# Optimization experiments

Hardware: AMD Instinct MI355X
Metric: run time of the kernel (lower is better)

Reference implementation:

```python
import jax, jax.numpy as jnp
import numpy as np

N, E, F_IN, H, L = 1536, 49152, 27, 64, 32


def _ln(x, g, b, eps=1e-5):
    m = x.mean(-1, keepdims=True)
    v = ((x - m) ** 2).mean(-1, keepdims=True)
    return (x - m) * jax.lax.rsqrt(v + eps) * g + b


def _gatv2(x, src, dst, Wl, bl, Wr, br, att, bias, n):
    # PyG GATv2Conv, heads=1: alpha_ij = softmax_j( att . leaky_relu(Wl x_j + Wr x_i) )
    xl = x @ Wl + bl  # source transform [n,H]
    xr = x @ Wr + br  # target transform [n,H]
    e = jax.nn.leaky_relu(xl[src] + xr[dst], 0.2)  # [E',H]
    s = e @ att  # [E'] attention logits
    m = jax.ops.segment_max(s, dst, num_segments=n)
    w = jnp.exp(s - m[dst])
    denom = jax.ops.segment_sum(w, dst, num_segments=n)
    alpha = w / denom[dst]
    return jax.ops.segment_sum(alpha[:, None] * xl[src], dst, num_segments=n) + bias


def _model(x, eps_nodes, eps_graph, edge_index,
           Wl1, bl1, Wr1, br1, att1, bias1,
           Wl2, bl2, Wr2, br2, att2, bias2,
           Wnm, bnm, Wnv, bnv, Wgm, bgm, Wgv, bgv,
           Wd1, bd1, ln1_g, ln1_b, Wd2, bd2, ln2_g, ln2_b, Wd3, bd3,
           We1, be1, lne_g, lne_b, We2, be2,
           Wf1, bf1, lnf_g, lnf_b, Wf2, bf2):
    n = x.shape[0]
    loop = jnp.arange(n)
    src = jnp.concatenate([edge_index[0], loop])  # add self loops (PyG default)
    dst = jnp.concatenate([edge_index[1], loop])
    h = jax.nn.relu(_gatv2(x, src, dst, Wl1, bl1, Wr1, br1, att1, bias1, n))
    h = jax.nn.relu(_gatv2(h, src, dst, Wl2, bl2, Wr2, br2, att2, bias2, n))
    node_mu = h @ Wnm + bnm
    node_logvar = h @ Wnv + bnv
    gh = h.mean(0)
    graph_mu = gh @ Wgm + bgm
    graph_logvar = gh @ Wgv + bgv
    z = node_mu + eps_nodes * jnp.exp(0.5 * node_logvar)  # node reparam (training)
    _zg = graph_mu + eps_graph * jnp.exp(0.5 * graph_logvar)  # z_graph: computed, unused downstream as in source
    # dec_node_features MLP
    nf = _ln(jax.nn.relu(z @ Wd1 + bd1), ln1_g, ln1_b)
    nf = _ln(jax.nn.relu(nf @ Wd2 + bd2), ln2_g, ln2_b)
    nf = nf @ Wd3 + bd3  # [n, F_IN]
    # feature_refinement (node_embeddings = h is passed in forward)
    nf = _ln(jax.nn.relu(jnp.concatenate([nf, h], -1) @ Wf1 + bf1), lnf_g, lnf_b)
    node_features = nf @ Wf2 + bf2
    # edge_pred over all i<j pairs, vectorized (replaces the O(N^2) python loop)
    iu, ju = jnp.triu_indices(n, k=1)
    ei = jnp.concatenate([z[iu], z[ju]], -1)  # [P, 2L]
    eh = _ln(jax.nn.relu(ei @ We1 + be1), lne_g, lne_b)
    edge_logits = (eh @ We2 + be2)[:, 0]  # [P]
    return node_features, edge_logits, node_mu, node_logvar, graph_mu, graph_logvar


def setup_inputs() -> dict:
    key = jax.random.key(0)
    ki = iter(jax.random.split(key, 40))
    def W(fi, fo):
        return jax.random.normal(next(ki), (fi, fo), jnp.float32) / np.sqrt(fi)
    z64 = jnp.zeros((H,), jnp.float32)
    o64 = jnp.ones((H,), jnp.float32)
    zL = jnp.zeros((L,), jnp.float32)
    zF = jnp.zeros((F_IN,), jnp.float32)
    inp = {}
    inp["x"] = jax.random.normal(next(ki), (N, F_IN), jnp.float32)
    inp["edge_index"] = jax.random.randint(next(ki), (2, E), 0, N)
    inp["eps_nodes"] = jax.random.normal(next(ki), (N, L), jnp.float32)
    inp["eps_graph"] = jax.random.normal(next(ki), (L,), jnp.float32)
    inp.update(Wl1=W(F_IN, H), bl1=z64, Wr1=W(F_IN, H), br1=z64,
               att1=jax.random.normal(next(ki), (H,), jnp.float32) / np.sqrt(H), bias1=z64,
               Wl2=W(H, H), bl2=z64, Wr2=W(H, H), br2=z64,
               att2=jax.random.normal(next(ki), (H,), jnp.float32) / np.sqrt(H), bias2=z64)
    inp.update(Wnm=W(H, L), bnm=zL, Wnv=W(H, L), bnv=zL,
               Wgm=W(H, L), bgm=zL, Wgv=W(H, L), bgv=zL)
    inp.update(Wd1=W(L, H), bd1=z64, ln1_g=o64, ln1_b=z64,
               Wd2=W(H, H), bd2=z64, ln2_g=o64, ln2_b=z64,
               Wd3=W(H, F_IN), bd3=zF)
    inp.update(We1=W(2 * L, H), be1=z64, lne_g=o64, lne_b=z64,
               We2=W(H, 1), be2=jnp.zeros((1,), jnp.float32))
    inp.update(Wf1=W(F_IN + H, H), bf1=z64, lnf_g=o64, lnf_b=z64,
               Wf2=W(H, F_IN), bf2=zF)
    return inp


def reference(x, edge_index, eps_nodes, eps_graph,
              Wl1, bl1, Wr1, br1, att1, bias1,
              Wl2, bl2, Wr2, br2, att2, bias2,
              Wnm, bnm, Wnv, bnv, Wgm, bgm, Wgv, bgv,
              Wd1, bd1, ln1_g, ln1_b, Wd2, bd2, ln2_g, ln2_b, Wd3, bd3,
              We1, be1, lne_g, lne_b, We2, be2,
              Wf1, bf1, lnf_g, lnf_b, Wf2, bf2):
    return _model(x, eps_nodes, eps_graph, edge_index,
                  Wl1, bl1, Wr1, br1, att1, bias1,
                  Wl2, bl2, Wr2, br2, att2, bias2,
                  Wnm, bnm, Wnv, bnv, Wgm, bgm, Wgv, bgv,
                  Wd1, bd1, ln1_g, ln1_b, Wd2, bd2, ln2_g, ln2_b, Wd3, bd3,
                  We1, be1, lne_g, lne_b, We2, be2,
                  Wf1, bf1, lnf_g, lnf_b, Wf2, bf2)
```

## Files before the change

### kernel.cpp

```cpp
#include <hip/hip_runtime.h>

#define NN 1536
#define NE 49152
#define NM (NE + NN)
#define FIN 27
#define HD 64
#define LDIM 32
#define PP 1178880

#define EL_OFF  (NN*FIN)
#define MU_OFF  (EL_OFF + PP)
#define LV_OFF  (MU_OFF + NN*LDIM)
#define GMU_OFF (LV_OFF + NN*LDIM)
#define GLV_OFF (GMU_OFF + LDIM)

#define EP_BLOCKS 1024

__device__ __forceinline__ float wsum(float v) {
#pragma unroll
  for (int m = 1; m < 64; m <<= 1) v += __shfl_xor(v, m, 64);
  return v;
}
__device__ __forceinline__ void wsum2(float& a, float& b) {
#pragma unroll
  for (int m = 1; m < 64; m <<= 1) {
    a += __shfl_xor(a, m, 64);
    b += __shfl_xor(b, m, 64);
  }
}
__device__ __forceinline__ float lnorm64(float x, float g, float b) {
  float s1 = x, s2 = x * x;
  wsum2(s1, s2);
  float mu = s1 * (1.0f / 64.0f);
  float var = fmaf(-mu, mu, s2 * (1.0f / 64.0f));
  return (x - mu) * rsqrtf(var + 1e-5f) * g + b;
}
__device__ __forceinline__ void cp4(float* dst, const float* __restrict__ src,
                                    int n4, int t) {
  const float4* s4 = (const float4*)src;
  float4* d4 = (float4*)dst;
  for (int e = t; e < n4; e += 256) d4[e] = s4[e];
}

template <int KIN, bool FUSE, bool ZERO>
__global__ __launch_bounds__(256) void gvae_xform(
    const float* __restrict__ in, const float* __restrict__ Dn,
    const float* __restrict__ hbias,
    const float* __restrict__ Wl, const float* __restrict__ bl,
    const float* __restrict__ Wr, const float* __restrict__ br,
    float* __restrict__ xl, float* __restrict__ xr,
    float* __restrict__ zbase, int nz4) {
  __shared__ __align__(16) float sWl[KIN * HD];
  __shared__ __align__(16) float sWr[KIN * HD];
  int t = threadIdx.x;
  if (ZERO) {
    float4 zz = {0.f, 0.f, 0.f, 0.f};
    float4* z4 = (float4*)zbase;
    for (int e = blockIdx.x * 256 + t; e < nz4; e += (NN / 4) * 256) z4[e] = zz;
  }
  cp4(sWl, Wl, KIN * 16, t);
  cp4(sWr, Wr, KIN * 16, t);
  int i = blockIdx.x * 4 + (t >> 6);
  int k = t & 63;
  float xv = (k < KIN) ? in[i * KIN + k] : 0.f;
  if (FUSE) xv = fmaxf(xv / Dn[i] + hbias[k], 0.f);
  float l0 = bl[k], l1 = 0.f, r0 = br[k], r1 = 0.f;
  __syncthreads();
#pragma unroll
  for (int a = 0; a < KIN; a += 2) {
    float xa = __shfl(xv, a, 64);
    l0 = fmaf(xa, sWl[a * HD + k], l0);
    r0 = fmaf(xa, sWr[a * HD + k], r0);
    if (a + 1 < KIN) {
      float xb = __shfl(xv, a + 1, 64);
      l1 = fmaf(xb, sWl[(a + 1) * HD + k], l1);
      r1 = fmaf(xb, sWr[(a + 1) * HD + k], r1);
    }
  }
  xl[i * HD + k] = l0 + l1;
  xr[i * HD + k] = r0 + r1;
}

__global__ __launch_bounds__(256) void gvae_edgepass(
    const int* __restrict__ ei,
    const float* __restrict__ xl, const float* __restrict__ xr,
    const float* __restrict__ att,
    float* __restrict__ A, float* __restrict__ D) {
  int wid = blockIdx.x * 4 + (threadIdx.x >> 6);
  int lane = threadIdx.x & 63;
  const int NW = EP_BLOCKS * 4;
  float ak = att[lane];
#pragma unroll 2
  for (int m = wid; m < NM; m += NW) {
    int src, dst;
    if (m < NE) { src = ei[m]; dst = ei[NE + m]; }
    else        { src = m - NE; dst = src; }
    float xls = xl[src * HD + lane];
    float e = xls + xr[dst * HD + lane];
    e = fmaxf(e, 0.2f * e);
    float w = expf(wsum(e * ak));
    atomicAdd(&A[dst * HD + lane], w * xls);
    if (lane == 0) atomicAdd(&D[dst], w);
  }
}

#define oE1 0
#define oD1 4096
#define oD2 6144
#define oF1 10240
#define SWTOT 16064

__global__ __launch_bounds__(256, 2) void gvae_node(
    const float* __restrict__ A2, const float* __restrict__ D2,
    const float* __restrict__ bias2,
    const float* __restrict__ eps,
    const float* __restrict__ Wnm, const float* __restrict__ bnm,
    const float* __restrict__ Wnv, const float* __restrict__ bnv,
    const float* __restrict__ We1, const float* __restrict__ be1,
    const float* __restrict__ Wd1, const float* __restrict__ bd1,
    const float* __restrict__ g1, const float* __restrict__ b1,
    const float* __restrict__ Wd2, const float* __restrict__ bd2,
    const float* __restrict__ g2, const float* __restrict__ b2,
    const float* __restrict__ Wd3, const float* __restrict__ bd3,
    const float* __restrict__ Wf1, const float* __restrict__ bf1,
    const float* __restrict__ gf, const float* __restrict__ bfv,
    const float* __restrict__ Wf2, const float* __restrict__ bf2,
    float* __restrict__ uo, float* __restrict__ vo,
    float* __restrict__ gh, float* __restrict__ out) {
  __shared__ __align__(16) float sW[SWTOT];
  __shared__ float ghred[256];
  int t = threadIdx.x;
  cp4(sW + oE1, We1, 1024, t);
  cp4(sW + oD1, Wd1, 512, t);
  cp4(sW + oD2, Wd2, 1024, t);
  cp4(sW + oF1, Wf1, 1456, t);

  int i = blockIdx.x * 4 + (t >> 6);
  int k = t & 63;
  int kk = k & 31;
  int kc = (k < FIN) ? k : (FIN - 1);
  float h2k = fmaxf(A2[i * HD + k] / D2[i] + bias2[k], 0.f);
  ghred[t] = h2k;
  __syncthreads();
  if (t < 64) {
    float s = (ghred[t] + ghred[t + 64]) + (ghred[t + 128] + ghred[t + 192]);
    atomicAdd(&gh[t], s * (1.0f / NN));
  }

  const float* W = (k < 32) ? Wnm : Wnv;
  float c0 = (k < 32) ? bnm[kk] : bnv[kk];
  float c1 = 0.f, c2 = 0.f, c3 = 0.f;
#pragma unroll
  for (int a = 0; a < HD; a += 4) {
    c0 = fmaf(__shfl(h2k, a, 64),     W[a * LDIM + kk],       c0);
    c1 = fmaf(__shfl(h2k, a + 1, 64), W[(a + 1) * LDIM + kk], c1);
    c2 = fmaf(__shfl(h2k, a + 2, 64), W[(a + 2) * LDIM + kk], c2);
    c3 = fmaf(__shfl(h2k, a + 3, 64), W[(a + 3) * LDIM + kk], c3);
  }
  float acc = (c0 + c1) + (c2 + c3);
  if (k < 32) out[MU_OFF + i * LDIM + kk] = acc;
  else        out[LV_OFF + i * LDIM + kk] = acc;

  float lv = __shfl(acc, k + 32, 64);
  float zk = acc + eps[i * LDIM + kk] * expf(0.5f * lv);

  float u0 = be1[k], u1 = 0.f, v0 = 0.f, v1 = 0.f;
#pragma unroll
  for (int a = 0; a < LDIM; a += 2) {
    float za = __shfl(zk, a, 64);
    float zb = __shfl(zk, a + 1, 64);
    u0 = fmaf(za, sW[oE1 + a * HD + k], u0);
    u1 = fmaf(zb, sW[oE1 + (a + 1) * HD + k], u1);
    v0 = fmaf(za, sW[oE1 + (a + LDIM) * HD + k], v0);
    v1 = fmaf(zb, sW[oE1 + (a + 1 + LDIM) * HD + k], v1);
  }
  uo[i * HD + k] = u0 + u1;
  vo[i * HD + k] = v0 + v1;

  c0 = bd1[k]; c1 = 0.f; c2 = 0.f; c3 = 0.f;
#pragma unroll
  for (int a = 0; a < LDIM; a += 4) {
    c0 = fmaf(__shfl(zk, a, 64),     sW[oD1 + a * HD + k],       c0);
    c1 = fmaf(__shfl(zk, a + 1, 64), sW[oD1 + (a + 1) * HD + k], c1);
    c2 = fmaf(__shfl(zk, a + 2, 64), sW[oD1 + (a + 2) * HD + k], c2);
    c3 = fmaf(__shfl(zk, a + 3, 64), sW[oD1 + (a + 3) * HD + k], c3);
  }
  float nf1 = lnorm64(fmaxf((c0 + c1) + (c2 + c3), 0.f), g1[k], b1[k]);

  c0 = bd2[k]; c1 = 0.f; c2 = 0.f; c3 = 0.f;
#pragma unroll
  for (int a = 0; a < HD; a += 4) {
    c0 = fmaf(__shfl(nf1, a, 64),     sW[oD2 + a * HD + k],       c0);
    c1 = fmaf(__shfl(nf1, a + 1, 64), sW[oD2 + (a + 1) * HD + k], c1);
    c2 = fmaf(__shfl(nf1, a + 2, 64), sW[oD2 + (a + 2) * HD + k], c2);
    c3 = fmaf(__shfl(nf1, a + 3, 64), sW[oD2 + (a + 3) * HD + k], c3);
  }
  float nf2 = lnorm64(fmaxf((c0 + c1) + (c2 + c3), 0.f), g2[k], b2[k]);

  c0 = 0.f; c1 = 0.f; c2 = 0.f; c3 = 0.f;
#pragma unroll
  for (int a = 0; a < HD; a += 4) {
    c0 = fmaf(__shfl(nf2, a, 64),     Wd3[a * FIN + kc],       c0);
    c1 = fmaf(__shfl(nf2, a + 1, 64), Wd3[(a + 1) * FIN + kc], c1);
    c2 = fmaf(__shfl(nf2, a + 2, 64), Wd3[(a + 2) * FIN + kc], c2);
    c3 = fmaf(__shfl(nf2, a + 3, 64), Wd3[(a + 3) * FIN + kc], c3);
  }
  float nf3 = (k < FIN) ? ((c0 + c1) + (c2 + c3) + bd3[kc]) : 0.f;

  c0 = bf1[k]; c1 = 0.f; c2 = 0.f; c3 = 0.f;
#pragma unroll
  for (int j = 0; j < FIN; j++) {
    float nj = __shfl(nf3, j, 64);
    c0 = fmaf(nj, sW[oF1 + j * HD + k], c0);
  }
#pragma unroll
  for (int a = 0; a < HD; a += 4) {
    c0 = fmaf(__shfl(h2k, a, 64),     sW[oF1 + (FIN + a) * HD + k],     c0);
    c1 = fmaf(__shfl(h2k, a + 1, 64), sW[oF1 + (FIN + a + 1) * HD + k], c1);
    c2 = fmaf(__shfl(h2k, a + 2, 64), sW[oF1 + (FIN + a + 2) * HD + k], c2);
    c3 = fmaf(__shfl(h2k, a + 3, 64), sW[oF1 + (FIN + a + 3) * HD + k], c3);
  }
  float rr = lnorm64(fmaxf((c0 + c1) + (c2 + c3), 0.f), gf[k], bfv[k]);

  c0 = 0.f; c1 = 0.f; c2 = 0.f; c3 = 0.f;
#pragma unroll
  for (int a = 0; a < HD; a += 4) {
    c0 = fmaf(__shfl(rr, a, 64),     Wf2[a * FIN + kc],       c0);
    c1 = fmaf(__shfl(rr, a + 1, 64), Wf2[(a + 1) * FIN + kc], c1);
    c2 = fmaf(__shfl(rr, a + 2, 64), Wf2[(a + 2) * FIN + kc], c2);
    c3 = fmaf(__shfl(rr, a + 3, 64), Wf2[(a + 3) * FIN + kc], c3);
  }
  if (k < FIN) out[i * FIN + k] = (c0 + c1) + (c2 + c3) + bf2[kc];
}

__global__ __launch_bounds__(256) void gvae_edge(
    const float* __restrict__ u, const float* __restrict__ v,
    const float* __restrict__ lng, const float* __restrict__ lnb,
    const float* __restrict__ w2, const float* __restrict__ be2,
    const float* __restrict__ gh,
    const float* __restrict__ Wgm, const float* __restrict__ bgm,
    const float* __restrict__ Wgv, const float* __restrict__ bgv,
    float* __restrict__ out) {
  __shared__ float U[64 * 64];
  __shared__ float V[64 * 68];
  __shared__ float C[64];
  __shared__ float cc[2];
  int t = threadIdx.x;
  int wv = t >> 6, lane = t & 63;

  if (blockIdx.x == 0 && wv == 3) {
    int kk = lane & 31;
    float ghk = gh[lane];
    const float* W = (lane < 32) ? Wgm : Wgv;
    float c0 = (lane < 32) ? bgm[kk] : bgv[kk];
    float c1 = 0.f, c2 = 0.f, c3 = 0.f;
#pragma unroll
    for (int a = 0; a < HD; a += 4) {
      c0 = fmaf(__shfl(ghk, a, 64),     W[a * LDIM + kk],       c0);
      c1 = fmaf(__shfl(ghk, a + 1, 64), W[(a + 1) * LDIM + kk], c1);
      c2 = fmaf(__shfl(ghk, a + 2, 64), W[(a + 2) * LDIM + kk], c2);
      c3 = fmaf(__shfl(ghk, a + 3, 64), W[(a + 3) * LDIM + kk], c3);
    }
    float acc = (c0 + c1) + (c2 + c3);
    if (lane < 32) out[GMU_OFF + kk] = acc;
    else           out[GLV_OFF + kk] = acc;
  }

  int rem = blockIdx.x, bi = 0;
  while (rem >= 24 - bi) { rem -= 24 - bi; bi++; }
  int bj = bi + rem;

  const float4* u4p = (const float4*)(u + bi * 64 * HD);
  const float4* v4p = (const float4*)(v + bj * 64 * HD);
#pragma unroll
  for (int it = 0; it < 4; ++it) {
    int r = t + it * 256;
    int row = r >> 4, q = r & 15;
    float4 uu = u4p[r];
    *(float4*)&U[row * 64 + q * 4] = uu;
    float4 vv = v4p[r];
    *(float4*)&V[row * 68 + q * 4] = vv;
  }
  if (t < 64) {
    float ck = lng[t] * w2[t];
    C[t] = ck;
    float cb = lnb[t] * w2[t];
    float sC = wsum(ck);
    float sB = wsum(cb);
    if (t == 0) { cc[0] = sC; cc[1] = sB + be2[0]; }
  }
  __syncthreads();
  float C1 = cc[0], C0 = cc[1];

  float S1[16], S2[16], Sc[16];
#pragma unroll
  for (int ii = 0; ii < 16; ii++) { S1[ii] = 0.f; S2[ii] = 0.f; Sc[ii] = 0.f; }
  const float* Ub = &U[(wv * 16) * 64];
  for (int k4 = 0; k4 < 16; k4++) {
    float4 v4 = *(const float4*)&V[lane * 68 + k4 * 4];
    float4 c4 = *(const float4*)&C[k4 * 4];
#pragma unroll
    for (int ii = 0; ii < 16; ii++) {
      float4 u4 = *(const float4*)&Ub[ii * 64 + k4 * 4];
      float t0 = fmaxf(u4.x + v4.x, 0.f);
      float t1 = fmaxf(u4.y + v4.y, 0.f);
      float t2 = fmaxf(u4.z + v4.z, 0.f);
      float t3 = fmaxf(u4.w + v4.w, 0.f);
      S1[ii] += (t0 + t1) + (t2 + t3);
      S2[ii] = fmaf(t0, t0, fmaf(t1, t1, fmaf(t2, t2, fmaf(t3, t3, S2[ii]))));
      Sc[ii] = fmaf(t0, c4.x, fmaf(t1, c4.y, fmaf(t2, c4.z, fmaf(t3, c4.w, Sc[ii]))));
    }
  }
  int j = bj * 64 + lane;
  const float inv64 = 1.0f / 64.0f;
#pragma unroll
  for (int ii = 0; ii < 16; ii++) {
    int i = bi * 64 + wv * 16 + ii;
    if (j > i) {
      int pbase = i * (2 * NN - i - 1) / 2 - i - 1;
      float mu = S1[ii] * inv64;
      float var = fmaf(-mu, mu, S2[ii] * inv64);
      float logit = (Sc[ii] - mu * C1) * rsqrtf(var + 1e-5f) + C0;
      out[EL_OFF + pbase + j] = logit;
    }
  }
}

extern "C" void kernel_launch(void* const* d_in, const int* in_sizes, int n_in,
                              void* d_out, int out_size, void* d_ws, size_t ws_size,
                              hipStream_t stream) {
  const float* x    = (const float*)d_in[0];
  const int*   ei   = (const int*)d_in[1];
  const float* eps  = (const float*)d_in[2];
  const float* Wl1  = (const float*)d_in[4];
  const float* bl1  = (const float*)d_in[5];
  const float* Wr1  = (const float*)d_in[6];
  const float* br1  = (const float*)d_in[7];
  const float* att1 = (const float*)d_in[8];
  const float* bias1= (const float*)d_in[9];
  const float* Wl2  = (const float*)d_in[10];
  const float* bl2  = (const float*)d_in[11];
  const float* Wr2  = (const float*)d_in[12];
  const float* br2  = (const float*)d_in[13];
  const float* att2 = (const float*)d_in[14];
  const float* bias2= (const float*)d_in[15];
  const float* Wnm  = (const float*)d_in[16];
  const float* bnm  = (const float*)d_in[17];
  const float* Wnv  = (const float*)d_in[18];
  const float* bnv  = (const float*)d_in[19];
  const float* Wgm  = (const float*)d_in[20];
  const float* bgm  = (const float*)d_in[21];
  const float* Wgv  = (const float*)d_in[22];
  const float* bgv  = (const float*)d_in[23];
  const float* Wd1  = (const float*)d_in[24];
  const float* bd1  = (const float*)d_in[25];
  const float* ln1g = (const float*)d_in[26];
  const float* ln1b = (const float*)d_in[27];
  const float* Wd2  = (const float*)d_in[28];
  const float* bd2  = (const float*)d_in[29];
  const float* ln2g = (const float*)d_in[30];
  const float* ln2b = (const float*)d_in[31];
  const float* Wd3  = (const float*)d_in[32];
  const float* bd3  = (const float*)d_in[33];
  const float* We1  = (const float*)d_in[34];
  const float* be1  = (const float*)d_in[35];
  const float* lneg = (const float*)d_in[36];
  const float* lneb = (const float*)d_in[37];
  const float* We2  = (const float*)d_in[38];
  const float* be2  = (const float*)d_in[39];
  const float* Wf1  = (const float*)d_in[40];
  const float* bf1  = (const float*)d_in[41];
  const float* lnfg = (const float*)d_in[42];
  const float* lnfb = (const float*)d_in[43];
  const float* Wf2  = (const float*)d_in[44];
  const float* bf2  = (const float*)d_in[45];
  float* out = (float*)d_out;

  float* fb  = (float*)d_ws;
  float* xl1 = fb;
  float* xr1 = xl1 + NN * HD;
  float* xl2 = xr1 + NN * HD;
  float* xr2 = xl2 + NN * HD;
  float* uu  = xr2 + NN * HD;
  float* vv  = uu  + NN * HD;
  float* A1  = vv  + NN * HD;
  float* A2  = A1  + NN * HD;
  float* D1  = A2  + NN * HD;
  float* D2  = D1  + NN;
  float* gh  = D2  + NN;
  int nz4 = (2 * NN * HD + 2 * NN + HD) / 4;

  gvae_xform<FIN, false, true><<<NN / 4, 256, 0, stream>>>(
      x, nullptr, nullptr, Wl1, bl1, Wr1, br1, xl1, xr1, A1, nz4);
  gvae_edgepass<<<EP_BLOCKS, 256, 0, stream>>>(ei, xl1, xr1, att1, A1, D1);
  gvae_xform<HD, true, false><<<NN / 4, 256, 0, stream>>>(
      A1, D1, bias1, Wl2, bl2, Wr2, br2, xl2, xr2, nullptr, 0);
  gvae_edgepass<<<EP_BLOCKS, 256, 0, stream>>>(ei, xl2, xr2, att2, A2, D2);

  gvae_node<<<NN / 4, 256, 0, stream>>>(A2, D2, bias2, eps,
      Wnm, bnm, Wnv, bnv, We1, be1,
      Wd1, bd1, ln1g, ln1b, Wd2, bd2, ln2g, ln2b, Wd3, bd3,
      Wf1, bf1, lnfg, lnfb, Wf2, bf2,
      uu, vv, gh, out);
  gvae_edge<<<300, 256, 0, stream>>>(uu, vv, lneg, lneb, We2, be2,
                                     gh, Wgm, bgm, Wgv, bgv, out);
}
```

Baseline: 257.6 us.

## Replace atomic edge scatter with CSR gather-based GAT aggregation fused into node kernels

Builds a CSR (count, scan, scatter) of incoming edges per destination node, including self-loops. Each node's wave then gathers its neighbours' xl, computes attention weights and the normalised aggregate in registers. The gather is fused into the layer-2 transform kernel and into the node MLP kernel. This removes the per-lane float atomics into A/D, the zeroing pass and the separate edge-pass kernels. In exchange it adds three small CSR-construction kernels, including a single-block scan, plus a serial per-node edge loop whose length depends on degree balance.

```diff
diff --git a/kernel.cpp b/kernel.cpp
--- a/kernel.cpp
+++ b/kernel.cpp
@@ -14,8 +14,6 @@
 #define GMU_OFF (LV_OFF + NN*LDIM)
 #define GLV_OFF (GMU_OFF + LDIM)
 
-#define EP_BLOCKS 1024
-
 __device__ __forceinline__ float wsum(float v) {
 #pragma unroll
   for (int m = 1; m < 64; m <<= 1) v += __shfl_xor(v, m, 64);
@@ -42,36 +40,64 @@
   for (int e = t; e < n4; e += 256) d4[e] = s4[e];
 }
 
-template <int KIN, bool FUSE, bool ZERO>
-__global__ __launch_bounds__(256) void gvae_xform(
-    const float* __restrict__ in, const float* __restrict__ Dn,
-    const float* __restrict__ hbias,
+__device__ __forceinline__ float gat_gather(const int* __restrict__ rowptr,
+                                            const int* __restrict__ slot,
+                                            const float* __restrict__ xl,
+                                            float xri, float ak, int i, int k) {
+  int beg = rowptr[i], end = rowptr[i + 1];
+  float acc = 0.f, den = 0.f;
+  for (int e0 = beg; e0 < end; e0 += 64) {
+    int sidx = (e0 + k < end) ? slot[e0 + k] : 0;
+    int nn = min(64, end - e0);
+    int j = 0;
+    for (; j + 1 < nn; j += 2) {
+      int s0 = __shfl(sidx, j, 64), s1 = __shfl(sidx, j + 1, 64);
+      float x0 = xl[s0 * HD + k], x1 = xl[s1 * HD + k];
+      float e0v = x0 + xri, e1v = x1 + xri;
+      e0v = fmaxf(e0v, 0.2f * e0v);
+      e1v = fmaxf(e1v, 0.2f * e1v);
+      float p0 = e0v * ak, p1 = e1v * ak;
+      wsum2(p0, p1);
+      float w0 = expf(p0), w1 = expf(p1);
+      acc = fmaf(w0, x0, acc); den += w0;
+      acc = fmaf(w1, x1, acc); den += w1;
+    }
+    if (j < nn) {
+      int s0 = __shfl(sidx, j, 64);
+      float x0 = xl[s0 * HD + k];
+      float e0v = x0 + xri;
+      e0v = fmaxf(e0v, 0.2f * e0v);
+      float w0 = expf(wsum(e0v * ak));
+      acc = fmaf(w0, x0, acc); den += w0;
+    }
+  }
+  return acc / den;
+}
+
+__global__ __launch_bounds__(256) void gvae_xform1(
+    const float* __restrict__ in,
     const float* __restrict__ Wl, const float* __restrict__ bl,
     const float* __restrict__ Wr, const float* __restrict__ br,
     float* __restrict__ xl, float* __restrict__ xr,
-    float* __restrict__ zbase, int nz4) {
-  __shared__ __align__(16) float sWl[KIN * HD];
-  __shared__ __align__(16) float sWr[KIN * HD];
+    const int* __restrict__ ei, int* __restrict__ cnt) {
+  __shared__ __align__(16) float sWl[FIN * HD];
+  __shared__ __align__(16) float sWr[FIN * HD];
   int t = threadIdx.x;
-  if (ZERO) {
-    float4 zz = {0.f, 0.f, 0.f, 0.f};
-    float4* z4 = (float4*)zbase;
-    for (int e = blockIdx.x * 256 + t; e < nz4; e += (NN / 4) * 256) z4[e] = zz;
-  }
-  cp4(sWl, Wl, KIN * 16, t);
-  cp4(sWr, Wr, KIN * 16, t);
+  int gid = blockIdx.x * 256 + t;
+  if (gid < NE) atomicAdd(&cnt[ei[NE + gid]], 1);
+  cp4(sWl, Wl, FIN * 16, t);
+  cp4(sWr, Wr, FIN * 16, t);
   int i = blockIdx.x * 4 + (t >> 6);
   int k = t & 63;
-  float xv = (k < KIN) ? in[i * KIN + k] : 0.f;
-  if (FUSE) xv = fmaxf(xv / Dn[i] + hbias[k], 0.f);
+  float xv = (k < FIN) ? in[i * FIN + k] : 0.f;
   float l0 = bl[k], l1 = 0.f, r0 = br[k], r1 = 0.f;
   __syncthreads();
 #pragma unroll
-  for (int a = 0; a < KIN; a += 2) {
+  for (int a = 0; a < FIN; a += 2) {
     float xa = __shfl(xv, a, 64);
     l0 = fmaf(xa, sWl[a * HD + k], l0);
     r0 = fmaf(xa, sWr[a * HD + k], r0);
-    if (a + 1 < KIN) {
+    if (a + 1 < FIN) {
       float xb = __shfl(xv, a + 1, 64);
       l1 = fmaf(xb, sWl[(a + 1) * HD + k], l1);
       r1 = fmaf(xb, sWr[(a + 1) * HD + k], r1);
@@ -81,27 +107,76 @@
   xr[i * HD + k] = r0 + r1;
 }
 
-__global__ __launch_bounds__(256) void gvae_edgepass(
-    const int* __restrict__ ei,
+__global__ __launch_bounds__(256) void gvae_scan(
+    const int* __restrict__ cnt, int* __restrict__ rowptr,
+    int* __restrict__ cursor, int* __restrict__ slot) {
+  __shared__ int part[256];
+  int t = threadIdx.x;
+  int base = t * 6;
+  int v[6];
+  int s = 0;
+#pragma unroll
+  for (int j = 0; j < 6; j++) { v[j] = cnt[base + j] + 1; s += v[j]; }
+  part[t] = s;
+  __syncthreads();
+  for (int off = 1; off < 256; off <<= 1) {
+    int y = (t >= off) ? part[t - off] : 0;
+    __syncthreads();
+    part[t] += y;
+    __syncthreads();
+  }
+  int r = part[t] - s;
+#pragma unroll
+  for (int j = 0; j < 6; j++) {
+    int node = base + j;
+    rowptr[node] = r;
+    slot[r] = node;
+    cursor[node] = r + 1;
+    r += v[j];
+  }
+  if (t == 255) rowptr[NN] = r;
+}
+
+__global__ __launch_bounds__(256) void gvae_scatter(
+    const int* __restrict__ ei, int* __restrict__ cursor, int* __restrict__ slot) {
+  int m = blockIdx.x * 256 + threadIdx.x;
+  if (m < NE) {
+    int d = ei[NE + m];
+    int p = atomicAdd(&cursor[d], 1);
+    slot[p] = ei[m];
+  }
+}
+
+__global__ __launch_bounds__(256) void gvae_gatherx(
+    const int* __restrict__ rowptr, const int* __restrict__ slot,
     const float* __restrict__ xl, const float* __restrict__ xr,
-    const float* __restrict__ att,
-    float* __restrict__ A, float* __restrict__ D) {
-  int wid = blockIdx.x * 4 + (threadIdx.x >> 6);
-  int lane = threadIdx.x & 63;
-  const int NW = EP_BLOCKS * 4;
-  float ak = att[lane];
-#pragma unroll 2
-  for (int m = wid; m < NM; m += NW) {
-    int src, dst;
-    if (m < NE) { src = ei[m]; dst = ei[NE + m]; }
-    else        { src = m - NE; dst = src; }
-    float xls = xl[src * HD + lane];
-    float e = xls + xr[dst * HD + lane];
-    e = fmaxf(e, 0.2f * e);
-    float w = expf(wsum(e * ak));
-    atomicAdd(&A[dst * HD + lane], w * xls);
-    if (lane == 0) atomicAdd(&D[dst], w);
-  }
+    const float* __restrict__ att, const float* __restrict__ hbias,
+    const float* __restrict__ Wl, const float* __restrict__ bl,
+    const float* __restrict__ Wr, const float* __restrict__ br,
+    float* __restrict__ xlo, float* __restrict__ xro) {
+  __shared__ __align__(16) float sWl[HD * HD];
+  __shared__ __align__(16) float sWr[HD * HD];
+  int t = threadIdx.x;
+  cp4(sWl, Wl, HD * 16, t);
+  cp4(sWr, Wr, HD * 16, t);
+  int i = blockIdx.x * 4 + (t >> 6);
+  int k = t & 63;
+  float xri = xr[i * HD + k];
+  float ak = att[k];
+  float hv = fmaxf(gat_gather(rowptr, slot, xl, xri, ak, i, k) + hbias[k], 0.f);
+  float l0 = bl[k], l1 = 0.f, r0 = br[k], r1 = 0.f;
+  __syncthreads();
+#pragma unroll
+  for (int a = 0; a < HD; a += 2) {
+    float xa = __shfl(hv, a, 64);
+    float xb = __shfl(hv, a + 1, 64);
+    l0 = fmaf(xa, sWl[a * HD + k], l0);
+    r0 = fmaf(xa, sWr[a * HD + k], r0);
+    l1 = fmaf(xb, sWl[(a + 1) * HD + k], l1);
+    r1 = fmaf(xb, sWr[(a + 1) * HD + k], r1);
+  }
+  xlo[i * HD + k] = l0 + l1;
+  xro[i * HD + k] = r0 + r1;
 }
 
 #define oE1 0
@@ -111,8 +186,9 @@
 #define SWTOT 16064
 
 __global__ __launch_bounds__(256, 2) void gvae_node(
-    const float* __restrict__ A2, const float* __restrict__ D2,
-    const float* __restrict__ bias2,
+    const int* __restrict__ rowptr, const int* __restrict__ slot,
+    const float* __restrict__ xl, const float* __restrict__ xr,
+    const float* __restrict__ att, const float* __restrict__ bias2,
     const float* __restrict__ eps,
     const float* __restrict__ Wnm, const float* __restrict__ bnm,
     const float* __restrict__ Wnv, const float* __restrict__ bnv,
@@ -139,7 +215,10 @@
   int k = t & 63;
   int kk = k & 31;
   int kc = (k < FIN) ? k : (FIN - 1);
-  float h2k = fmaxf(A2[i * HD + k] / D2[i] + bias2[k], 0.f);
+
+  float xri = xr[i * HD + k];
+  float ak = att[k];
+  float h2k = fmaxf(gat_gather(rowptr, slot, xl, xri, ak, i, k) + bias2[k], 0.f);
   ghred[t] = h2k;
   __syncthreads();
   if (t < 64) {
@@ -278,8 +357,8 @@
     int row = r >> 4, q = r & 15;
     float4 uu = u4p[r];
     *(float4*)&U[row * 64 + q * 4] = uu;
-    float4 vv = v4p[r];
-    *(float4*)&V[row * 68 + q * 4] = vv;
+    float4 vvv = v4p[r];
+    *(float4*)&V[row * 68 + q * 4] = vvv;
   }
   if (t < 64) {
     float ck = lng[t] * w2[t];
@@ -383,21 +462,20 @@
   float* xr2 = xl2 + NN * HD;
   float* uu  = xr2 + NN * HD;
   float* vv  = uu  + NN * HD;
-  float* A1  = vv  + NN * HD;
-  float* A2  = A1  + NN * HD;
-  float* D1  = A2  + NN * HD;
-  float* D2  = D1  + NN;
-  float* gh  = D2  + NN;
-  int nz4 = (2 * NN * HD + 2 * NN + HD) / 4;
-
-  gvae_xform<FIN, false, true><<<NN / 4, 256, 0, stream>>>(
-      x, nullptr, nullptr, Wl1, bl1, Wr1, br1, xl1, xr1, A1, nz4);
-  gvae_edgepass<<<EP_BLOCKS, 256, 0, stream>>>(ei, xl1, xr1, att1, A1, D1);
-  gvae_xform<HD, true, false><<<NN / 4, 256, 0, stream>>>(
-      A1, D1, bias1, Wl2, bl2, Wr2, br2, xl2, xr2, nullptr, 0);
-  gvae_edgepass<<<EP_BLOCKS, 256, 0, stream>>>(ei, xl2, xr2, att2, A2, D2);
-
-  gvae_node<<<NN / 4, 256, 0, stream>>>(A2, D2, bias2, eps,
+  float* gh  = vv  + NN * HD;
+  int* cnt    = (int*)(gh + HD);
+  int* rowptr = cnt + NN;
+  int* cursor = rowptr + NN + 1;
+  int* slot   = cursor + NN;
+
+  hipMemsetAsync(gh, 0, (HD + NN) * sizeof(float), stream);
+
+  gvae_xform1<<<NN / 4, 256, 0, stream>>>(x, Wl1, bl1, Wr1, br1, xl1, xr1, ei, cnt);
+  gvae_scan<<<1, 256, 0, stream>>>(cnt, rowptr, cursor, slot);
+  gvae_scatter<<<NE / 256, 256, 0, stream>>>(ei, cursor, slot);
+  gvae_gatherx<<<NN / 4, 256, 0, stream>>>(rowptr, slot, xl1, xr1, att1, bias1,
+                                           Wl2, bl2, Wr2, br2, xl2, xr2);
+  gvae_node<<<NN / 4, 256, 0, stream>>>(rowptr, slot, xl2, xr2, att2, bias2, eps,
       Wnm, bnm, Wnv, bnv, We1, be1,
       Wd1, bd1, ln1g, ln1b, Wd2, bd2, ln2g, ln2b, Wd3, bd3,
       Wf1, bf1, lnfg, lnfb, Wf2, bf2,
```

New measurement: 242.2 us. 1.06x faster.
